# Performance work log

Measured on AMD Instinct MI355X. Metric: run time of the kernel, lower is better.

The kernel has to match this reference:

```python
import math
import jax, jax.numpy as jnp
import numpy as np
from jax import lax

B, L, C_IN = 8, 1024, 64
D_MODEL, N_HEADS, D_FF, E_LAYERS, FACTOR = 512, 8, 2048, 3, 5


def conv1d_circ(x, w):
    # x [B,L,Cin], w [Cout,Cin,K]; torch Conv1d with padding_mode='circular'
    pad = (w.shape[-1] - 1) // 2
    xp = jnp.pad(x, ((0, 0), (pad, pad), (0, 0)), mode='wrap')
    return lax.conv_general_dilated(xp, jnp.transpose(w, (2, 1, 0)), (1,), 'VALID',
                                    dimension_numbers=('NWC', 'WIO', 'NWC'))


def pos_emb(Lq, d):
    pos = jnp.arange(Lq, dtype=jnp.float32)[:, None]
    div = jnp.exp(jnp.arange(0, d, 2, dtype=jnp.float32) * (-math.log(10000.0) / d))
    pe = jnp.zeros((Lq, d), dtype=jnp.float32)
    pe = pe.at[:, 0::2].set(jnp.sin(pos * div)).at[:, 1::2].set(jnp.cos(pos * div))
    return pe


def layer_norm(x, g, b, eps=1e-5):
    m = x.mean(-1, keepdims=True)
    v = ((x - m) ** 2).mean(-1, keepdims=True)
    return (x - m) / jnp.sqrt(v + eps) * g + b


def prob_attention(Q, K, V, rkey):
    # ProbSparse self-attention (mask_flag=False). Q,K,V: [B,H,L,D]
    Bq, H, Lq, D = Q.shape
    U = min(FACTOR * int(math.ceil(math.log(Lq))), Lq)  # sample_k == n_top since L_Q == L_K
    idx = jax.random.randint(rkey, (Lq, U), 0, Lq)       # per-query sampled key indices
    Ks = jnp.take(K, idx, axis=2)                        # [B,H,L,U,D]
    QKs = jnp.einsum('bhld,bhlud->bhlu', Q, Ks)          # sampled scores
    M = QKs.max(-1) - QKs.sum(-1) / Lq                   # sparsity measure (sum / L_K)
    _, top = lax.top_k(M, U)                             # [B,H,U] top-u query indices
    Qr = jnp.take_along_axis(Q, top[..., None], axis=2)  # [B,H,U,D]
    scores = jnp.einsum('bhud,bhld->bhul', Qr, K) * (1.0 / math.sqrt(D))
    attn = jax.nn.softmax(scores, axis=-1)
    upd = jnp.einsum('bhul,bhld->bhud', attn, V)
    # initial context = mean of V broadcast over queries; scatter updates at top-u
    ctx = jnp.broadcast_to(V.mean(axis=2, keepdims=True), (Bq, H, Lq, D))
    bi = jnp.arange(Bq)[:, None, None]
    hi = jnp.arange(H)[None, :, None]
    ctx = ctx.at[bi, hi, top].set(upd)
    return ctx


def attn_block(x, Wq, bq, Wk, bk, Wv, bv, Wo, bo, rkey):
    Bq, Lq, Dm = x.shape
    Dh = Dm // N_HEADS
    q = (x @ Wq.T + bq).reshape(Bq, Lq, N_HEADS, Dh).transpose(0, 2, 1, 3)
    k = (x @ Wk.T + bk).reshape(Bq, Lq, N_HEADS, Dh).transpose(0, 2, 1, 3)
    v = (x @ Wv.T + bv).reshape(Bq, Lq, N_HEADS, Dh).transpose(0, 2, 1, 3)
    ctx = prob_attention(q, k, v, rkey)
    out = ctx.transpose(0, 2, 1, 3).reshape(Bq, Lq, Dm)
    return out @ Wo.T + bo


def distil_conv(x, w, b, g, be):
    # Conv1d(k=3, circular) -> BatchNorm1d (batch stats) -> ELU -> MaxPool1d(3,2,1)
    y = conv1d_circ(x, w) + b
    mu = y.mean((0, 1))
    var = ((y - mu) ** 2).mean((0, 1))
    y = (y - mu) / jnp.sqrt(var + 1e-5) * g + be
    y = jax.nn.elu(y)
    y = lax.reduce_window(y, -jnp.inf, lax.max, (1, 3, 1), (1, 2, 1),
                          ((0, 0), (1, 1), (0, 0)))
    return y


def forward(x_enc, tok_w, Wq, bq, Wk, bk, Wv, bv, Wo, bo, c1w, c1b, c2w, c2b,
            n1g, n1b, n2g, n2b, dcw, dcb, bng, bnb, fng, fnb):
    x = x_enc + 1e-10
    x = conv1d_circ(x, tok_w) + pos_emb(x.shape[1], D_MODEL)  # embedding (dropout=0)
    for l in range(E_LAYERS):
        rkey = jax.random.fold_in(jax.random.key(42), l)
        x = x + attn_block(x, Wq[l], bq[l], Wk[l], bk[l], Wv[l], bv[l], Wo[l], bo[l], rkey)
        y = x = layer_norm(x, n1g[l], n1b[l])
        y = jax.nn.relu(y @ c1w[l].T + c1b[l])   # Conv1d k=1 == linear
        y = y @ c2w[l].T + c2b[l]
        x = layer_norm(x + y, n2g[l], n2b[l])
        if l < E_LAYERS - 1:
            x = distil_conv(x, dcw[l], dcb[l], bng[l], bnb[l])
    x = layer_norm(x, fng, fnb)
    return x.mean(axis=1)  # [B, D_MODEL]


def setup_inputs() -> dict:
    key = jax.random.key(0)
    ks = jax.random.split(key, 12)
    s = 0.02
    E = E_LAYERS
    return {
        'x_enc': jax.random.normal(ks[0], (B, L, C_IN), jnp.float32),
        'tok_w': jax.random.normal(ks[1], (D_MODEL, C_IN, 3), jnp.float32) * s,
        'Wq': jax.random.normal(ks[2], (E, D_MODEL, D_MODEL), jnp.float32) * s,
        'bq': jnp.zeros((E, D_MODEL), jnp.float32),
        'Wk': jax.random.normal(ks[3], (E, D_MODEL, D_MODEL), jnp.float32) * s,
        'bk': jnp.zeros((E, D_MODEL), jnp.float32),
        'Wv': jax.random.normal(ks[4], (E, D_MODEL, D_MODEL), jnp.float32) * s,
        'bv': jnp.zeros((E, D_MODEL), jnp.float32),
        'Wo': jax.random.normal(ks[5], (E, D_MODEL, D_MODEL), jnp.float32) * s,
        'bo': jnp.zeros((E, D_MODEL), jnp.float32),
        'c1w': jax.random.normal(ks[6], (E, D_FF, D_MODEL), jnp.float32) * s,
        'c1b': jnp.zeros((E, D_FF), jnp.float32),
        'c2w': jax.random.normal(ks[7], (E, D_MODEL, D_FF), jnp.float32) * s,
        'c2b': jnp.zeros((E, D_MODEL), jnp.float32),
        'n1g': jnp.ones((E, D_MODEL), jnp.float32),
        'n1b': jnp.zeros((E, D_MODEL), jnp.float32),
        'n2g': jnp.ones((E, D_MODEL), jnp.float32),
        'n2b': jnp.zeros((E, D_MODEL), jnp.float32),
        'dcw': jax.random.normal(ks[8], (E - 1, D_MODEL, D_MODEL, 3), jnp.float32) * s,
        'dcb': jnp.zeros((E - 1, D_MODEL), jnp.float32),
        'bng': jnp.ones((E - 1, D_MODEL), jnp.float32),
        'bnb': jnp.zeros((E - 1, D_MODEL), jnp.float32),
        'fng': jnp.ones((D_MODEL,), jnp.float32),
        'fnb': jnp.zeros((D_MODEL,), jnp.float32),
    }


def reference(x_enc, tok_w, Wq, bq, Wk, bk, Wv, bv, Wo, bo, c1w, c1b, c2w, c2b,
              n1g, n1b, n2g, n2b, dcw, dcb, bng, bnb, fng, fnb):
    return forward(x_enc, tok_w, Wq, bq, Wk, bk, Wv, bv, Wo, bo, c1w, c1b, c2w, c2b,
                   n1g, n1b, n2g, n2b, dcw, dcb, bng, bnb, fng, fnb)
```

## Files before the change

kernel.cpp:

```cpp
#include <hip/hip_runtime.h>
#include <hip/hip_bf16.h>
#include <math.h>

typedef __hip_bfloat16 bf16;
typedef short bf16x8 __attribute__((ext_vector_type(8)));
typedef float f32x4 __attribute__((ext_vector_type(4)));

__device__ inline short f2bs(float x) {
  bf16 h = __float2bfloat16(x);
  return *reinterpret_cast<short*>(&h);
}

__device__ inline void threefry2x32(unsigned k0, unsigned k1,
                                    unsigned x0, unsigned x1,
                                    unsigned& o0, unsigned& o1) {
  unsigned ks[3] = {k0, k1, k0 ^ k1 ^ 0x1BD11BDAu};
  const int rot[2][4] = {{13, 15, 26, 6}, {17, 29, 16, 24}};
  x0 += ks[0];
  x1 += ks[1];
  #pragma unroll
  for (int i = 0; i < 5; i++) {
    const int* r = rot[i & 1];
    #pragma unroll
    for (int j = 0; j < 4; j++) {
      x0 += x1;
      x1 = (x1 << r[j]) | (x1 >> (32 - r[j]));
      x1 ^= x0;
    }
    x0 += ks[(i + 1) % 3];
    x1 += ks[(i + 2) % 3] + (unsigned)(i + 1);
  }
  o0 = x0;
  o1 = x1;
}

__global__ void idx_kernel(int* __restrict__ idx, int L, int U, int layer) {
  int total = L * U, half = total / 2;
  int i = blockIdx.x * blockDim.x + threadIdx.x;
  if (i >= half) return;
  unsigned k0, k1;
  threefry2x32(0u, 42u, 0u, (unsigned)layer, k0, k1);
  unsigned o0, o1;
  threefry2x32(k0, k1, (unsigned)i, (unsigned)(half + i), o0, o1);
  idx[i] = (int)(o0 & (unsigned)(L - 1));
  idx[half + i] = (int)(o1 & (unsigned)(L - 1));
}

__global__ __launch_bounds__(256) void bgemm_pad(
    const bf16* __restrict__ A, const bf16* __restrict__ W,
    const float* __restrict__ bias, const float* __restrict__ R, int rmod,
    float* __restrict__ C, bf16* __restrict__ Cb,
    int M, int N, int K, int relu, int outmode) {
  constexpr int LS = 40;
  __shared__ bf16 As[64 * LS];
  __shared__ bf16 Ws[64 * LS];
  int tid = threadIdx.x;
  int lane = tid & 63, w = tid >> 6;
  size_t row0 = (size_t)blockIdx.x * 64, col0 = (size_t)blockIdx.y * 64;
  int srow = (w << 4) + (lane >> 2);
  int scol = (lane & 3) << 3;
  const bf16* ag = A + (row0 + srow) * K + scol;
  const bf16* wg = W + (col0 + srow) * K + scol;
  int wb = srow * LS + scol;
  int wr = (w >> 1) << 5, wc = (w & 1) << 5;
  int fr = lane & 15, fk = (lane >> 4) << 3;
  f32x4 acc[2][2] = {};
  bf16x8 ra = *(const bf16x8*)ag;
  bf16x8 rw = *(const bf16x8*)wg;
  for (int k0 = 0; k0 < K; k0 += 32) {
    __syncthreads();
    *(bf16x8*)(As + wb) = ra;
    *(bf16x8*)(Ws + wb) = rw;
    if (k0 + 32 < K) {
      ag += 32; wg += 32;
      ra = *(const bf16x8*)ag;
      rw = *(const bf16x8*)wg;
    }
    __syncthreads();
    bf16x8 af[2], bfv[2];
    #pragma unroll
    for (int m = 0; m < 2; m++)
      af[m] = *(const bf16x8*)(As + (wr + m * 16 + fr) * LS + fk);
    #pragma unroll
    for (int n = 0; n < 2; n++)
      bfv[n] = *(const bf16x8*)(Ws + (wc + n * 16 + fr) * LS + fk);
    #pragma unroll
    for (int m = 0; m < 2; m++)
      #pragma unroll
      for (int n = 0; n < 2; n++)
        acc[m][n] = __builtin_amdgcn_mfma_f32_16x16x32_bf16(af[m], bfv[n], acc[m][n], 0, 0, 0);
  }
  int cr = (lane >> 4) << 2;
  int cc0 = lane & 15;
  #pragma unroll
  for (int m = 0; m < 2; m++) {
    #pragma unroll
    for (int n = 0; n < 2; n++) {
      #pragma unroll
      for (int r = 0; r < 4; r++) {
        size_t rr = row0 + wr + m * 16 + cr + r;
        size_t cc = col0 + wc + n * 16 + cc0;
        float v = acc[m][n][r];
        if (bias) v += bias[cc];
        if (R) v += rmod ? R[(rr % rmod) * N + cc] : R[rr * N + cc];
        if (relu) v = fmaxf(v, 0.f);
        if (outmode != 2) C[rr * N + cc] = v;
        if (outmode) Cb[rr * N + cc] = __float2bfloat16(v);
      }
    }
  }
}

__global__ void castw_kernel(const float* __restrict__ wq, const float* __restrict__ wk,
                             const float* __restrict__ wv, const float* __restrict__ wo,
                             const float* __restrict__ c1, const float* __restrict__ c2,
                             bf16* __restrict__ wqkv, bf16* __restrict__ wob,
                             bf16* __restrict__ c1b, bf16* __restrict__ c2b) {
  int i = blockIdx.x * 256 + threadIdx.x;
  if (i >= 786432) return;
  const float* s;
  bf16* d;
  int j;
  if (i < 196608) {
    s = (i < 65536) ? wq : (i < 131072) ? wk : wv;
    float4 v = ((const float4*)s)[i & 65535];
    d = wqkv + (size_t)i * 4;
    d[0] = __float2bfloat16(v.x); d[1] = __float2bfloat16(v.y);
    d[2] = __float2bfloat16(v.z); d[3] = __float2bfloat16(v.w);
    return;
  }
  if (i < 262144) { s = wo; j = i - 196608; d = wob + (size_t)j * 4; }
  else if (i < 524288) { s = c1; j = i - 262144; d = c1b + (size_t)j * 4; }
  else { s = c2; j = i - 524288; d = c2b + (size_t)j * 4; }
  float4 v = ((const float4*)s)[j];
  d[0] = __float2bfloat16(v.x); d[1] = __float2bfloat16(v.y);
  d[2] = __float2bfloat16(v.z); d[3] = __float2bfloat16(v.w);
}

__global__ void catb3_kernel(const float* __restrict__ a, const float* __restrict__ b,
                             const float* __restrict__ c, float* __restrict__ d) {
  int i = blockIdx.x * 256 + threadIdx.x;
  if (i >= 1536) return;
  d[i] = (i < 512) ? a[i] : (i < 1024) ? b[i - 512] : c[i - 1024];
}

__global__ void wperm_kernel(const float* __restrict__ w, bf16* __restrict__ wcol) {
  int i = blockIdx.x * 256 + threadIdx.x;
  if (i >= 512 * 1536) return;
  int o = i / 1536, r = i % 1536, k = r / 512, c = r % 512;
  wcol[i] = __float2bfloat16(w[o * 1536 + c * 3 + k]);
}

__global__ void tokperm_kernel(const float* __restrict__ w, bf16* __restrict__ d) {
  int i = blockIdx.x * 256 + threadIdx.x;
  if (i >= 512 * 192) return;
  int o = i / 192, r = i % 192, k = r / 64, c = r % 64;
  d[i] = __float2bfloat16(w[o * 192 + c * 3 + k]);
}

__global__ void pe_kernel(float* __restrict__ PE) {
  int t = blockIdx.x, o = threadIdx.x;
  int i2 = o >> 1;
  float div = expf((float)(2 * i2) * (-9.210340371976184f / 512.f));
  float ang = (float)t * div;
  PE[t * 512 + o] = (o & 1) ? cosf(ang) : sinf(ang);
}

__global__ void im2col_e_kernel(const float* __restrict__ x, bf16* __restrict__ d,
                                int B, int L) {
  size_t i = (size_t)blockIdx.x * 256 + threadIdx.x;
  if (i >= (size_t)B * L * 192) return;
  int j = (int)(i % 192);
  size_t row = i / 192;
  int k = j >> 6, c = j & 63;
  int t = (int)(row % L), b = (int)(row / L);
  int ts = (t - 1 + k) & (L - 1);
  d[i] = __float2bfloat16(x[((size_t)(b * L + ts)) * 64 + c] + 1e-10f);
}

__global__ __launch_bounds__(256) void sparsity_kernel(
    const float* __restrict__ QKV, const int* __restrict__ idx,
    float* __restrict__ M, int B, int H, int L, int U) {
  int tpb = L >> 2;
  int xcd = blockIdx.x & 7, slot = blockIdx.x >> 3;
  int bh = xcd + ((slot / tpb) << 3);
  int tb = slot % tpb;
  int wave = threadIdx.x >> 6;
  int t = tb * 4 + wave;
  int lane = threadIdx.x & 63;
  int h = bh & 7, b = bh >> 3;
  int ul = lane >> 3;
  int j = lane & 7;
  const float* qrow = QKV + ((size_t)(b * L + t)) * 1536 + h * 64 + j * 8;
  float4 qa = *(const float4*)qrow;
  float4 qb = *(const float4*)(qrow + 4);
  const float* kbase = QKV + (size_t)b * L * 1536 + 512 + h * 64 + j * 8;
  const int* irow = idx + t * U;
  float mx = -INFINITY, sm = 0.f;
  int iters = (U + 7) >> 3;
  for (int i = 0; i < iters; i++) {
    int u = i * 8 + ul;
    bool valid = (u < U);
    int kt = valid ? irow[u] : 0;
    const float* kr = kbase + (size_t)kt * 1536;
    float4 ka = *(const float4*)kr;
    float4 kb = *(const float4*)(kr + 4);
    float part = qa.x * ka.x + qa.y * ka.y + qa.z * ka.z + qa.w * ka.w +
                 qb.x * kb.x + qb.y * kb.y + qb.z * kb.z + qb.w * kb.w;
    #pragma unroll
    for (int off = 1; off < 8; off <<= 1) part += __shfl_xor(part, off);
    if (valid) { mx = fmaxf(mx, part); sm += part; }
  }
  #pragma unroll
  for (int off = 8; off < 64; off <<= 1) {
    mx = fmaxf(mx, __shfl_xor(mx, off));
    sm += __shfl_xor(sm, off);
  }
  if (lane == 0) M[(size_t)bh * L + t] = mx - sm / (float)L;
}

__global__ __launch_bounds__(1024) void topk_kernel(
    const float* __restrict__ M, int* __restrict__ top, int L, int U) {
  __shared__ float wv[16];
  __shared__ int wi[16];
  __shared__ int best_s;
  int bh = blockIdx.x, tid = threadIdx.x;
  int lane = tid & 63, w = tid >> 6;
  float v = (tid < L) ? M[(size_t)bh * L + tid] : -INFINITY;
  int myt = tid;
  for (int it = 0; it < U; it++) {
    float bv = v;
    int bi = myt;
    #pragma unroll
    for (int off = 32; off; off >>= 1) {
      float ov = __shfl_xor(bv, off);
      int oi = __shfl_xor(bi, off);
      if (ov > bv || (ov == bv && oi < bi)) { bv = ov; bi = oi; }
    }
    if (lane == 0) { wv[w] = bv; wi[w] = bi; }
    __syncthreads();
    if (w == 0) {
      float v2 = (lane < 16) ? wv[lane] : -INFINITY;
      int i2 = (lane < 16) ? wi[lane] : 0x7fffffff;
      #pragma unroll
      for (int off = 8; off; off >>= 1) {
        float ov = __shfl_xor(v2, off);
        int oi = __shfl_xor(i2, off);
        if (ov > v2 || (ov == v2 && oi < i2)) { v2 = ov; i2 = oi; }
      }
      if (lane == 0) { best_s = i2; top[bh * U + it] = i2; }
    }
    __syncthreads();
    if (myt == best_s) v = -INFINITY;
  }
}

__global__ __launch_bounds__(512) void vmean_part_kernel(
    const float* __restrict__ QKV, float* __restrict__ VP, int L, int segs) {
  int b = blockIdx.x, s = blockIdx.y, c = threadIdx.x;
  int per = L / segs;
  const float* vb = QKV + ((size_t)(b * L + s * per)) * 1536 + 1024 + c;
  float acc = 0.f;
  for (int t = 0; t < per; t++) acc += vb[(size_t)t * 1536];
  VP[((size_t)(b * segs + s)) * 512 + c] = acc;
}

__global__ void vmean_reduce_kernel(const float* __restrict__ VP, float* __restrict__ Vmean,
                                    int segs, int L) {
  int i = blockIdx.x * 256 + threadIdx.x;
  if (i >= 8 * 512) return;
  int b = i >> 9, c = i & 511;
  float acc = 0.f;
  for (int s = 0; s < segs; s++) acc += VP[((size_t)(b * segs + s)) * 512 + c];
  Vmean[i] = acc / (float)L;
}

__global__ void bcast_ctx_kernel(const float* __restrict__ Vmean, bf16* __restrict__ ATTb,
                                 int B, int L) {
  size_t i = (size_t)blockIdx.x * 256 + threadIdx.x;
  if (i >= (size_t)B * L * 512) return;
  int c = (int)(i % 512);
  int b = (int)(i / ((size_t)512 * L));
  ATTb[i] = __float2bfloat16(Vmean[b * 512 + c]);
}

__global__ __launch_bounds__(256) void attn_mfma_kernel(
    const float* __restrict__ QKV, const int* __restrict__ top,
    bf16* __restrict__ ATTb, int B, int H, int L, int U) {
  __shared__ short q_lds[64 * 72];
  __shared__ short k_lds[64 * 72];
  __shared__ short vt_lds[64 * 72];
  __shared__ short p_lds[4][16 * 72];
  int bh = blockIdx.x;
  int h = bh & 7, b = bh >> 3;
  int tid = threadIdx.x;
  int lane = tid & 63, w = tid >> 6;
  int r = tid >> 2, q4 = tid & 3, c0 = q4 << 4;
  int fr = lane & 15, fk = (lane >> 4) << 3, g = lane >> 4;

  {
    short tmp[16];
    if (r < U) {
      int tq = top[bh * U + r];
      const float* src = QKV + ((size_t)(b * L + tq)) * 1536 + h * 64 + c0;
      #pragma unroll
      for (int i = 0; i < 4; i++) {
        float4 v = ((const float4*)src)[i];
        tmp[i * 4 + 0] = f2bs(v.x); tmp[i * 4 + 1] = f2bs(v.y);
        tmp[i * 4 + 2] = f2bs(v.z); tmp[i * 4 + 3] = f2bs(v.w);
      }
    } else {
      #pragma unroll
      for (int i = 0; i < 16; i++) tmp[i] = 0;
    }
    *(bf16x8*)&q_lds[r * 72 + c0] = *(bf16x8*)&tmp[0];
    *(bf16x8*)&q_lds[r * 72 + c0 + 8] = *(bf16x8*)&tmp[8];
  }
  __syncthreads();
  bf16x8 aq0 = *(const bf16x8*)&q_lds[(w * 16 + fr) * 72 + fk];
  bf16x8 aq1 = *(const bf16x8*)&q_lds[(w * 16 + fr) * 72 + 32 + fk];

  f32x4 ctx[4] = {};
  float m_run[4], l_run[4];
  #pragma unroll
  for (int i = 0; i < 4; i++) { m_run[i] = -INFINITY; l_run[i] = 0.f; }

  for (int t0 = 0; t0 < L; t0 += 64) {
    __syncthreads();
    {
      const float* ks = QKV + ((size_t)(b * L + t0 + r)) * 1536 + 512 + h * 64 + c0;
      const float* vs = ks + 512;
      short kt[16];
      #pragma unroll
      for (int i = 0; i < 4; i++) {
        float4 v = ((const float4*)ks)[i];
        kt[i * 4 + 0] = f2bs(v.x); kt[i * 4 + 1] = f2bs(v.y);
        kt[i * 4 + 2] = f2bs(v.z); kt[i * 4 + 3] = f2bs(v.w);
      }
      *(bf16x8*)&k_lds[r * 72 + c0] = *(bf16x8*)&kt[0];
      *(bf16x8*)&k_lds[r * 72 + c0 + 8] = *(bf16x8*)&kt[8];
      #pragma unroll
      for (int i = 0; i < 4; i++) {
        float4 v = ((const float4*)vs)[i];
        vt_lds[(c0 + i * 4 + 0) * 72 + r] = f2bs(v.x);
        vt_lds[(c0 + i * 4 + 1) * 72 + r] = f2bs(v.y);
        vt_lds[(c0 + i * 4 + 2) * 72 + r] = f2bs(v.z);
        vt_lds[(c0 + i * 4 + 3) * 72 + r] = f2bs(v.w);
      }
    }
    __syncthreads();
    f32x4 s[4];
    #pragma unroll
    for (int n = 0; n < 4; n++) {
      bf16x8 b0 = *(const bf16x8*)&k_lds[(n * 16 + fr) * 72 + fk];
      bf16x8 b1 = *(const bf16x8*)&k_lds[(n * 16 + fr) * 72 + 32 + fk];
      f32x4 z = {};
      z = __builtin_amdgcn_mfma_f32_16x16x32_bf16(aq0, b0, z, 0, 0, 0);
      s[n] = __builtin_amdgcn_mfma_f32_16x16x32_bf16(aq1, b1, z, 0, 0, 0);
    }
    #pragma unroll
    for (int n = 0; n < 4; n++)
      #pragma unroll
      for (int rg = 0; rg < 4; rg++) s[n][rg] *= 0.125f;
    #pragma unroll
    for (int rg = 0; rg < 4; rg++) {
      float tm = fmaxf(fmaxf(s[0][rg], s[1][rg]), fmaxf(s[2][rg], s[3][rg]));
      #pragma unroll
      for (int off = 1; off < 16; off <<= 1) tm = fmaxf(tm, __shfl_xor(tm, off));
      float mnew = fmaxf(m_run[rg], tm);
      float sc_old = expf(m_run[rg] - mnew);
      float rowsum = 0.f;
      #pragma unroll
      for (int n = 0; n < 4; n++) {
        float p = expf(s[n][rg] - mnew);
        s[n][rg] = p;
        rowsum += p;
      }
      #pragma unroll
      for (int off = 1; off < 16; off <<= 1) rowsum += __shfl_xor(rowsum, off);
      l_run[rg] = l_run[rg] * sc_old + rowsum;
      m_run[rg] = mnew;
      #pragma unroll
      for (int nd = 0; nd < 4; nd++) ctx[nd][rg] *= sc_old;
    }
    short* pw = p_lds[w];
    #pragma unroll
    for (int n = 0; n < 4; n++)
      #pragma unroll
      for (int rg = 0; rg < 4; rg++)
        pw[(g * 4 + rg) * 72 + n * 16 + fr] = f2bs(s[n][rg]);
    bf16x8 pa0 = *(const bf16x8*)&pw[fr * 72 + fk];
    bf16x8 pa1 = *(const bf16x8*)&pw[fr * 72 + 32 + fk];
    #pragma unroll
    for (int nd = 0; nd < 4; nd++) {
      bf16x8 v0 = *(const bf16x8*)&vt_lds[(nd * 16 + fr) * 72 + fk];
      bf16x8 v1 = *(const bf16x8*)&vt_lds[(nd * 16 + fr) * 72 + 32 + fk];
      ctx[nd] = __builtin_amdgcn_mfma_f32_16x16x32_bf16(pa0, v0, ctx[nd], 0, 0, 0);
      ctx[nd] = __builtin_amdgcn_mfma_f32_16x16x32_bf16(pa1, v1, ctx[nd], 0, 0, 0);
    }
  }
  #pragma unroll
  for (int rg = 0; rg < 4; rg++) {
    int qq = w * 16 + g * 4 + rg;
    if (qq < U) {
      int tq = top[bh * U + qq];
      float inv = 1.f / l_run[rg];
      #pragma unroll
      for (int nd = 0; nd < 4; nd++) {
        int d = nd * 16 + fr;
        ATTb[((size_t)(b * L + tq)) * 512 + h * 64 + d] =
            __float2bfloat16(ctx[nd][rg] * inv);
      }
    }
  }
}

__global__ __launch_bounds__(256) void ln_kernel(
    const float* __restrict__ Xin, const float* __restrict__ g,
    const float* __restrict__ bta, float* __restrict__ Xout,
    bf16* __restrict__ Xoutb, int rows) {
  __shared__ float part[8];
  int r = blockIdx.x, tid = threadIdx.x;
  int lane = tid & 63, w = tid >> 6;
  const float* xr = Xin + (size_t)r * 512;
  float v0 = xr[tid], v1 = xr[tid + 256];
  float s = v0 + v1;
  #pragma unroll
  for (int off = 1; off < 64; off <<= 1) s += __shfl_xor(s, off);
  if (lane == 0) part[w] = s;
  __syncthreads();
  float mean = (part[0] + part[1] + part[2] + part[3]) * (1.f / 512.f);
  float d0 = v0 - mean, d1 = v1 - mean;
  float q = d0 * d0 + d1 * d1;
  #pragma unroll
  for (int off = 1; off < 64; off <<= 1) q += __shfl_xor(q, off);
  if (lane == 0) part[4 + w] = q;
  __syncthreads();
  float var = (part[4] + part[5] + part[6] + part[7]) * (1.f / 512.f);
  float rs = rsqrtf(var + 1e-5f);
  float o0 = d0 * rs * g[tid] + bta[tid];
  float o1 = d1 * rs * g[tid + 256] + bta[tid + 256];
  float* out = Xout + (size_t)r * 512;
  out[tid] = o0;
  out[tid + 256] = o1;
  if (Xoutb) {
    Xoutb[(size_t)r * 512 + tid] = __float2bfloat16(o0);
    Xoutb[(size_t)r * 512 + tid + 256] = __float2bfloat16(o1);
  }
}

__global__ void im2col_kernel(const float* __restrict__ X, bf16* __restrict__ XCOL,
                              int B, int L) {
  size_t i = (size_t)blockIdx.x * 256 + threadIdx.x;
  size_t total = (size_t)B * L * 1536;
  if (i >= total) return;
  int c = (int)(i % 512);
  int k = (int)((i / 512) % 3);
  size_t row = i / 1536;
  int t = (int)(row % L), b = (int)(row / L);
  int ts = (t - 1 + k + L) % L;
  XCOL[i] = __float2bfloat16(X[((size_t)(b * L + ts)) * 512 + c]);
}

__global__ void zero_kernel(float* p, int n) {
  int i = blockIdx.x * 256 + threadIdx.x;
  if (i < n) p[i] = 0.f;
}

__global__ __launch_bounds__(256) void bnstat_kernel(
    const float* __restrict__ Y, float* __restrict__ acc, int rows) {
  int tid = threadIdx.x;
  int c0 = tid, c1 = tid + 256;
  float s0 = 0, s1 = 0, q0 = 0, q1 = 0;
  for (int r = blockIdx.x; r < rows; r += gridDim.x) {
    float v0 = Y[(size_t)r * 512 + c0];
    float v1 = Y[(size_t)r * 512 + c1];
    s0 += v0; q0 += v0 * v0;
    s1 += v1; q1 += v1 * v1;
  }
  atomicAdd(&acc[c0], s0);
  atomicAdd(&acc[c1], s1);
  atomicAdd(&acc[512 + c0], q0);
  atomicAdd(&acc[512 + c1], q1);
}

__global__ void bnpool_kernel(const float* __restrict__ Y, const float* __restrict__ acc,
                              const float* __restrict__ g, const float* __restrict__ be,
                              float* __restrict__ Xout, bf16* __restrict__ Xoutb,
                              int B, int L, int rows) {
  int Lout = L / 2;
  size_t i = (size_t)blockIdx.x * 256 + threadIdx.x;
  if (i >= (size_t)B * Lout * 512) return;
  int c = (int)(i % 512);
  size_t orow = i / 512;
  int to = (int)(orow % Lout), b = (int)(orow / Lout);
  float mu = acc[c] / (float)rows;
  float var = acc[512 + c] / (float)rows - mu * mu;
  float rs = rsqrtf(var + 1e-5f) * g[c];
  float mx = -INFINITY;
  #pragma unroll
  for (int dj = -1; dj <= 1; dj++) {
    int j = 2 * to + dj;
    if (j < 0 || j >= L) continue;
    float v = (Y[((size_t)(b * L + j)) * 512 + c] - mu) * rs + be[c];
    v = v > 0.f ? v : expm1f(v);
    mx = fmaxf(mx, v);
  }
  Xout[i] = mx;
  Xoutb[i] = __float2bfloat16(mx);
}

__global__ void meanrows_part_kernel(const float* __restrict__ Xin, float* __restrict__ MP,
                                     int L, int segs) {
  int b = blockIdx.x, s = blockIdx.y, d = threadIdx.x;
  int per = L / segs;
  const float* base = Xin + ((size_t)(b * L + s * per)) * 512 + d;
  float acc = 0.f;
  for (int t = 0; t < per; t++) acc += base[(size_t)t * 512];
  MP[((size_t)(b * segs + s)) * 512 + d] = acc;
}

__global__ void meanrows_red_kernel(const float* __restrict__ MP, float* __restrict__ out,
                                    int segs, int L) {
  int i = blockIdx.x * 256 + threadIdx.x;
  if (i >= 8 * 512) return;
  int b = i >> 9, c = i & 511;
  float acc = 0.f;
  for (int s = 0; s < segs; s++) acc += MP[((size_t)(b * segs + s)) * 512 + c];
  out[i] = acc / (float)L;
}

extern "C" void kernel_launch(void* const* d_in, const int* in_sizes, int n_in,
                              void* d_out, int out_size, void* d_ws, size_t ws_size,
                              hipStream_t stream) {
  const float* x_enc = (const float*)d_in[0];
  const float* tok_w = (const float*)d_in[1];
  const float* Wq = (const float*)d_in[2];
  const float* bq = (const float*)d_in[3];
  const float* Wk = (const float*)d_in[4];
  const float* bk = (const float*)d_in[5];
  const float* Wv = (const float*)d_in[6];
  const float* bv = (const float*)d_in[7];
  const float* Wo = (const float*)d_in[8];
  const float* bo = (const float*)d_in[9];
  const float* c1w = (const float*)d_in[10];
  const float* c1b = (const float*)d_in[11];
  const float* c2w = (const float*)d_in[12];
  const float* c2b = (const float*)d_in[13];
  const float* n1g = (const float*)d_in[14];
  const float* n1b = (const float*)d_in[15];
  const float* n2g = (const float*)d_in[16];
  const float* n2b = (const float*)d_in[17];
  const float* dcw = (const float*)d_in[18];
  const float* dcb = (const float*)d_in[19];
  const float* bng = (const float*)d_in[20];
  const float* bnb = (const float*)d_in[21];
  const float* fng = (const float*)d_in[22];
  const float* fnb = (const float*)d_in[23];

  const int B = 8, H = 8;
  const size_t NX = 4194304;

  float* ws = (float*)d_ws;
  float* X    = ws;
  float* XLN  = ws + NX;
  float* QKVf = ws + 2 * NX;
  bf16* H2b   = (bf16*)(ws + 2 * NX);
  float* Yc   = ws + 2 * NX;
  bf16* XCOLb = (bf16*)(ws + 4 * NX);
  bf16* INb   = (bf16*)(ws + 5 * NX);
  bf16* ATTb  = (bf16*)(ws + 5 * NX + NX / 2);
  float* WB   = ws + 6 * NX;
  bf16* WQKVb = (bf16*)(WB);
  bf16* Wob  = (bf16*)(WB + 393216);
  bf16* c1wb = (bf16*)(WB + 524288);
  bf16* c2wb = (bf16*)(WB + 1048576);
  bf16* wcvb = (bf16*)(WB + 1572864);
  bf16* tokwb = (bf16*)(WB + 1966080);
  float* PE   = WB + 2015232;
  float* MBUF = PE + 524288;
  float* VMEAN = MBUF + 65536;
  float* BNACC = VMEAN + 4096;
  int* IDX = (int*)(BNACC + 1024);
  int* TOP = IDX + 35840;
  float* VPART = (float*)(TOP + 2240);
  float* BQKV = VPART + 131072;

  pe_kernel<<<1024, 512, 0, stream>>>(PE);
  tokperm_kernel<<<(512 * 192 + 255) / 256, 256, 0, stream>>>(tok_w, tokwb);
  im2col_e_kernel<<<(int)(((size_t)B * 1024 * 192 + 255) / 256), 256, 0, stream>>>(
      x_enc, INb, B, 1024);
  bgemm_pad<<<dim3(128, 8), 256, 0, stream>>>(INb, tokwb, nullptr, PE, 1024,
                                              X, INb, 8192, 512, 192, 0, 1);

  int L = 1024;
  for (int l = 0; l < 3; l++) {
    int U = (L == 256) ? 30 : 35;
    int rows = B * L;
    dim3 g64(rows / 64, 8);

    castw_kernel<<<3072, 256, 0, stream>>>(
        Wq + (size_t)l * 262144, Wk + (size_t)l * 262144, Wv + (size_t)l * 262144,
        Wo + (size_t)l * 262144, c1w + (size_t)l * 1048576, c2w + (size_t)l * 1048576,
        WQKVb, Wob, c1wb, c2wb);
    catb3_kernel<<<6, 256, 0, stream>>>(bq + l * 512, bk + l * 512, bv + l * 512, BQKV);
    if (l < 2)
      wperm_kernel<<<3072, 256, 0, stream>>>(dcw + (size_t)l * 786432, wcvb);

    bgemm_pad<<<dim3(rows / 64, 24), 256, 0, stream>>>(
        INb, WQKVb, BQKV, nullptr, 0, QKVf, nullptr, rows, 1536, 512, 0, 0);

    int half = L * U / 2;
    idx_kernel<<<(half + 255) / 256, 256, 0, stream>>>(IDX, L, U, l);
    sparsity_kernel<<<(B * H * L) / 4, 256, 0, stream>>>(QKVf, IDX, MBUF, B, H, L, U);
    topk_kernel<<<B * H, 1024, 0, stream>>>(MBUF, TOP, L, U);
    vmean_part_kernel<<<dim3(B, 32), 512, 0, stream>>>(QKVf, VPART, L, 32);
    vmean_reduce_kernel<<<16, 256, 0, stream>>>(VPART, VMEAN, 32, L);
    bcast_ctx_kernel<<<(rows * 512) / 256, 256, 0, stream>>>(VMEAN, ATTb, B, L);
    attn_mfma_kernel<<<B * H, 256, 0, stream>>>(QKVf, TOP, ATTb, B, H, L, U);

    bgemm_pad<<<g64, 256, 0, stream>>>(ATTb, Wob, bo + l * 512, X, 0,
                                       X, nullptr, rows, 512, 512, 0, 0);
    ln_kernel<<<rows, 256, 0, stream>>>(X, n1g + l * 512, n1b + l * 512, XLN, INb, rows);
    bgemm_pad<<<dim3(rows / 64, 32), 256, 0, stream>>>(
        INb, c1wb, c1b + l * 2048, nullptr, 0, nullptr, H2b, rows, 2048, 512, 1, 2);
    bgemm_pad<<<g64, 256, 0, stream>>>(H2b, c2wb, c2b + l * 512, XLN, 0,
                                       X, nullptr, rows, 512, 2048, 0, 0);
    ln_kernel<<<rows, 256, 0, stream>>>(X, n2g + l * 512, n2b + l * 512, X, nullptr, rows);

    if (l < 2) {
      im2col_kernel<<<(int)(((size_t)rows * 1536) / 256), 256, 0, stream>>>(X, XCOLb, B, L);
      bgemm_pad<<<g64, 256, 0, stream>>>(XCOLb, wcvb, dcb + l * 512, nullptr, 0,
                                         Yc, nullptr, rows, 512, 1536, 0, 0);
      zero_kernel<<<4, 256, 0, stream>>>(BNACC, 1024);
      bnstat_kernel<<<128, 256, 0, stream>>>(Yc, BNACC, rows);
      bnpool_kernel<<<(rows / 2 * 512) / 256, 256, 0, stream>>>(
          Yc, BNACC, bng + l * 512, bnb + l * 512, X, INb, B, L, rows);
      L >>= 1;
    }
  }

  int rowsF = B * L;
  ln_kernel<<<rowsF, 256, 0, stream>>>(X, fng, fnb, XLN, nullptr, rowsF);
  meanrows_part_kernel<<<dim3(8, 8), 512, 0, stream>>>(XLN, VPART, L, 8);
  meanrows_red_kernel<<<16, 256, 0, stream>>>(VPART, (float*)d_out, 8, L);
}
```

Before: 900.7 us.

## Double-buffer GEMM tiles with direct global-to-LDS loads and XOR swizzle

Replaces the padded register-staged bf16 GEMM with a version that copies tiles straight from global memory into LDS using global_load_lds. It double-buffers 64-wide K tiles, so there is one barrier per K step and the next tile loads during the current MFMAs. An XOR swizzle replaces row padding to avoid LDS bank conflicts. The risk is correctness: the loads must complete before the barrier, and that waitcnt ordering is left implicit.

```diff
diff --git a/kernel.cpp b/kernel.cpp
--- a/kernel.cpp
+++ b/kernel.cpp
@@ -9,6 +9,12 @@
 __device__ inline short f2bs(float x) {
   bf16 h = __float2bfloat16(x);
   return *reinterpret_cast<short*>(&h);
+}
+
+__device__ inline void gload16(const bf16* g, bf16* l) {
+  __builtin_amdgcn_global_load_lds(
+      (const __attribute__((address_space(1))) unsigned int*)g,
+      (__attribute__((address_space(3))) unsigned int*)l, 16, 0, 0);
 }
 
 __device__ inline void threefry2x32(unsigned k0, unsigned k1,
@@ -46,49 +52,66 @@
   idx[half + i] = (int)(o1 & (unsigned)(L - 1));
 }
 
-__global__ __launch_bounds__(256) void bgemm_pad(
+__global__ __launch_bounds__(256) void bgemm_g(
     const bf16* __restrict__ A, const bf16* __restrict__ W,
     const float* __restrict__ bias, const float* __restrict__ R, int rmod,
     float* __restrict__ C, bf16* __restrict__ Cb,
     int M, int N, int K, int relu, int outmode) {
-  constexpr int LS = 40;
-  __shared__ bf16 As[64 * LS];
-  __shared__ bf16 Ws[64 * LS];
+  __shared__ bf16 As[2][64 * 64];
+  __shared__ bf16 Ws[2][64 * 64];
   int tid = threadIdx.x;
   int lane = tid & 63, w = tid >> 6;
   size_t row0 = (size_t)blockIdx.x * 64, col0 = (size_t)blockIdx.y * 64;
-  int srow = (w << 4) + (lane >> 2);
-  int scol = (lane & 3) << 3;
-  const bf16* ag = A + (row0 + srow) * K + scol;
-  const bf16* wg = W + (col0 + srow) * K + scol;
-  int wb = srow * LS + scol;
+  int srow = w * 16 + (lane >> 3);
+  int scol = (((lane & 7) ^ (lane >> 3)) << 4) >> 1;
+  const bf16* agA0 = A + (row0 + srow) * K + scol;
+  const bf16* agA1 = A + (row0 + srow + 8) * K + scol;
+  const bf16* agW0 = W + (col0 + srow) * K + scol;
+  const bf16* agW1 = W + (col0 + srow + 8) * K + scol;
+  int db0 = (w * 16) * 64;
+  int db1 = (w * 16 + 8) * 64;
   int wr = (w >> 1) << 5, wc = (w & 1) << 5;
-  int fr = lane & 15, fk = (lane >> 4) << 3;
+  int fr = lane & 15;
+  int fkb = ((lane >> 4) << 3) << 1;
   f32x4 acc[2][2] = {};
-  bf16x8 ra = *(const bf16x8*)ag;
-  bf16x8 rw = *(const bf16x8*)wg;
-  for (int k0 = 0; k0 < K; k0 += 32) {
+  int nt = K >> 6;
+  gload16(agA0, As[0] + db0); gload16(agA1, As[0] + db1);
+  gload16(agW0, Ws[0] + db0); gload16(agW1, Ws[0] + db1);
+  int cur = 0;
+  for (int t = 0; t < nt; t++) {
     __syncthreads();
-    *(bf16x8*)(As + wb) = ra;
-    *(bf16x8*)(Ws + wb) = rw;
-    if (k0 + 32 < K) {
-      ag += 32; wg += 32;
-      ra = *(const bf16x8*)ag;
-      rw = *(const bf16x8*)wg;
-    }
-    __syncthreads();
-    bf16x8 af[2], bfv[2];
+    if (t + 1 < nt) {
+      int ko = (t + 1) << 6;
+      gload16(agA0 + ko, As[cur ^ 1] + db0); gload16(agA1 + ko, As[cur ^ 1] + db1);
+      gload16(agW0 + ko, Ws[cur ^ 1] + db0); gload16(agW1 + ko, Ws[cur ^ 1] + db1);
+    }
+    const char* ab = (const char*)As[cur];
+    const char* wb = (const char*)Ws[cur];
+    bf16x8 af[2][2], bfv[2][2];
+    #pragma unroll
+    for (int m = 0; m < 2; m++) {
+      int row = wr + m * 16 + fr;
+      int xr = (row & 7) << 4;
+      #pragma unroll
+      for (int kk = 0; kk < 2; kk++)
+        af[m][kk] = *(const bf16x8*)(ab + row * 128 + ((fkb + kk * 64) ^ xr));
+    }
+    #pragma unroll
+    for (int n = 0; n < 2; n++) {
+      int row = wc + n * 16 + fr;
+      int xr = (row & 7) << 4;
+      #pragma unroll
+      for (int kk = 0; kk < 2; kk++)
+        bfv[n][kk] = *(const bf16x8*)(wb + row * 128 + ((fkb + kk * 64) ^ xr));
+    }
     #pragma unroll
     for (int m = 0; m < 2; m++)
-      af[m] = *(const bf16x8*)(As + (wr + m * 16 + fr) * LS + fk);
-    #pragma unroll
-    for (int n = 0; n < 2; n++)
-      bfv[n] = *(const bf16x8*)(Ws + (wc + n * 16 + fr) * LS + fk);
-    #pragma unroll
-    for (int m = 0; m < 2; m++)
-      #pragma unroll
-      for (int n = 0; n < 2; n++)
-        acc[m][n] = __builtin_amdgcn_mfma_f32_16x16x32_bf16(af[m], bfv[n], acc[m][n], 0, 0, 0);
+      #pragma unroll
+      for (int n = 0; n < 2; n++) {
+        acc[m][n] = __builtin_amdgcn_mfma_f32_16x16x32_bf16(af[m][0], bfv[n][0], acc[m][n], 0, 0, 0);
+        acc[m][n] = __builtin_amdgcn_mfma_f32_16x16x32_bf16(af[m][1], bfv[n][1], acc[m][n], 0, 0, 0);
+      }
+    cur ^= 1;
   }
   int cr = (lane >> 4) << 2;
   int cc0 = lane & 15;
@@ -590,8 +613,8 @@
   tokperm_kernel<<<(512 * 192 + 255) / 256, 256, 0, stream>>>(tok_w, tokwb);
   im2col_e_kernel<<<(int)(((size_t)B * 1024 * 192 + 255) / 256), 256, 0, stream>>>(
       x_enc, INb, B, 1024);
-  bgemm_pad<<<dim3(128, 8), 256, 0, stream>>>(INb, tokwb, nullptr, PE, 1024,
-                                              X, INb, 8192, 512, 192, 0, 1);
+  bgemm_g<<<dim3(128, 8), 256, 0, stream>>>(INb, tokwb, nullptr, PE, 1024,
+                                            X, INb, 8192, 512, 192, 0, 1);
 
   int L = 1024;
   for (int l = 0; l < 3; l++) {
@@ -607,7 +630,7 @@
     if (l < 2)
       wperm_kernel<<<3072, 256, 0, stream>>>(dcw + (size_t)l * 786432, wcvb);
 
-    bgemm_pad<<<dim3(rows / 64, 24), 256, 0, stream>>>(
+    bgemm_g<<<dim3(rows / 64, 24), 256, 0, stream>>>(
         INb, WQKVb, BQKV, nullptr, 0, QKVf, nullptr, rows, 1536, 512, 0, 0);
 
     int half = L * U / 2;
@@ -619,19 +642,19 @@
     bcast_ctx_kernel<<<(rows * 512) / 256, 256, 0, stream>>>(VMEAN, ATTb, B, L);
     attn_mfma_kernel<<<B * H, 256, 0, stream>>>(QKVf, TOP, ATTb, B, H, L, U);
 
-    bgemm_pad<<<g64, 256, 0, stream>>>(ATTb, Wob, bo + l * 512, X, 0,
-                                       X, nullptr, rows, 512, 512, 0, 0);
+    bgemm_g<<<g64, 256, 0, stream>>>(ATTb, Wob, bo + l * 512, X, 0,
+                                     X, nullptr, rows, 512, 512, 0, 0);
     ln_kernel<<<rows, 256, 0, stream>>>(X, n1g + l * 512, n1b + l * 512, XLN, INb, rows);
-    bgemm_pad<<<dim3(rows / 64, 32), 256, 0, stream>>>(
+    bgemm_g<<<dim3(rows / 64, 32), 256, 0, stream>>>(
         INb, c1wb, c1b + l * 2048, nullptr, 0, nullptr, H2b, rows, 2048, 512, 1, 2);
-    bgemm_pad<<<g64, 256, 0, stream>>>(H2b, c2wb, c2b + l * 512, XLN, 0,
-                                       X, nullptr, rows, 512, 2048, 0, 0);
+    bgemm_g<<<g64, 256, 0, stream>>>(H2b, c2wb, c2b + l * 512, XLN, 0,
+                                     X, nullptr, rows, 512, 2048, 0, 0);
     ln_kernel<<<rows, 256, 0, stream>>>(X, n2g + l * 512, n2b + l * 512, X, nullptr, rows);
 
     if (l < 2) {
       im2col_kernel<<<(int)(((size_t)rows * 1536) / 256), 256, 0, stream>>>(X, XCOLb, B, L);
-      bgemm_pad<<<g64, 256, 0, stream>>>(XCOLb, wcvb, dcb + l * 512, nullptr, 0,
-                                         Yc, nullptr, rows, 512, 1536, 0, 0);
+      bgemm_g<<<g64, 256, 0, stream>>>(XCOLb, wcvb, dcb + l * 512, nullptr, 0,
+                                       Yc, nullptr, rows, 512, 1536, 0, 0);
       zero_kernel<<<4, 256, 0, stream>>>(BNACC, 1024);
       bnstat_kernel<<<128, 256, 0, stream>>>(Yc, BNACC, rows);
       bnpool_kernel<<<(rows / 2 * 512) / 256, 256, 0, stream>>>(
```

Result: faster. 877.2 us (-2.6%).
